# Performance work log

Hardware: AMD Instinct MI355X
Metric: run time of the kernel (lower is better)

The kernel has to match this reference:

```python
import jax, jax.numpy as jnp
import numpy as np

B, S = 4, 8192
DIM, H = 1024, 8
C = 2 * H           # num_channels
E = DIM // C        # head_dim = 64
BASE, START, STRIDE = 10.0, 0, 1
CHUNK = 64
EPS = 1e-8
TWO_PI = 2.0 * np.pi


def setup_inputs() -> dict:
    key = jax.random.key(0)
    k1, k2, k3, k4, k5 = jax.random.split(key, 5)
    inputs = jax.random.normal(k1, (B, S, DIM), jnp.float32)
    timestamps = jnp.sort(jax.random.randint(k2, (B, S), 0, 8192, jnp.int32), axis=-1)
    next_timestamps = jnp.sort(jax.random.randint(k3, (B, S), 0, 8192, jnp.int32), axis=-1)
    mask = jnp.ones((B, S), dtype=bool)
    # learned parameters
    Wv = jax.random.normal(k4, (DIM, DIM), jnp.float32) / np.sqrt(DIM)  # proj_v.weight
    gamma_param = jnp.zeros((H,), jnp.float32)
    alpha = jax.random.normal(k5, (C,), jnp.float32) * 0.02
    beta = jnp.ones((C,), jnp.float32)
    return {"inputs": inputs, "Wv": Wv, "gamma_param": gamma_param, "alpha": alpha,
            "beta": beta, "timestamps": timestamps, "next_timestamps": next_timestamps,
            "mask": mask}


def chunkwise_recurrent_attention(q, k, v, decay_steps, mask, chunk):
    # q,k: [B,S,C,2]; v: [B,S,C,E]; decay_steps: [B,S,C]; mask: [B,S] bool
    b, s, c, d = q.shape
    e = v.shape[-1]
    m4 = mask[..., None, None].astype(q.dtype)
    q = q * m4
    k = k * m4
    v = v * m4
    decay = jnp.where(mask[..., None], decay_steps, jnp.ones_like(decay_steps))
    n = s // chunk

    def chunks(x):  # [B,S,...] -> [n,B,L,...]
        return x.reshape(b, n, chunk, *x.shape[2:]).swapaxes(0, 1)

    qc, kc, vc = chunks(q), chunks(k), chunks(v)
    dc = chunks(decay)                       # [n,B,L,C]
    mc = mask.reshape(b, n, chunk).swapaxes(0, 1)
    causal = jnp.tril(jnp.ones((chunk, chunk), q.dtype))

    def step(state, xs):
        qch, kch, vch, dch, mch = xs         # [B,L,C,2],[B,L,C,2],[B,L,C,E],[B,L,C],[B,L]
        prefix = jnp.cumprod(jnp.clip(dch, EPS), axis=1)            # [B,L,C]
        prev = jnp.einsum('blcd,bcde->blce', qch * prefix[..., None], state)
        dmat = prefix[:, :, None, :] / jnp.clip(prefix[:, None, :, :], EPS)  # [B,L,M,C]
        scores = jnp.einsum('blcd,bmcd->blmc', qch, kch)            # [B,L,M,C]
        weights = scores * dmat * causal[None, :, :, None]
        intra = jnp.einsum('blmc,bmce->blce', weights, vch)
        out = (prev + intra) * mch[..., None, None].astype(qch.dtype)
        plast = prefix[:, -1]                                       # [B,C]
        sw = plast[:, None, :] / jnp.clip(prefix, EPS)              # [B,L,C]
        new_state = state * plast[:, :, None, None] + \
            jnp.einsum('blcd,blce->bcde', kch * sw[..., None], vch)
        return new_state, out

    state0 = jnp.zeros((b, c, d, e), q.dtype)
    _, outs = jax.lax.scan(step, state0, (qc, kc, vc, dc, mc))
    return outs.swapaxes(0, 1).reshape(b, s, c, e)


def _forward(inputs, Wv, gamma_param, alpha, beta, timestamps, next_timestamps, mask):
    values = (inputs @ Wv.T).reshape(B, S, C, E)
    scales = jnp.arange(START, START + H * STRIDE, STRIDE, dtype=jnp.float32)
    intervals = jnp.power(BASE, scales).astype(jnp.int32).astype(jnp.float32)  # buffer cast to long
    scale_factor = TWO_PI * jnp.power(1.0 / BASE, scales)
    ts = timestamps.astype(jnp.float32)
    nts = next_timestamps.astype(jnp.float32)
    theta_k = jnp.remainder(ts[..., None], intervals) * scale_factor   # [B,S,H]
    theta_q = jnp.remainder(nts[..., None], intervals) * scale_factor
    key_ = jnp.stack((jnp.cos(theta_k), jnp.sin(theta_k)), axis=-1)    # [B,S,H,2]
    key_ = jnp.concatenate([key_, key_], axis=2)                       # [B,S,C,2]
    cos_q, sin_q = jnp.cos(theta_q), jnp.sin(theta_q)
    query = jnp.concatenate([jnp.stack((sin_q, -cos_q), -1),
                             jnp.stack((cos_q, sin_q), -1)], axis=2)   # [B,S,C,2]
    gamma = jax.nn.sigmoid(gamma_param)
    loggamma = jnp.log(jnp.clip(gamma, 1e-6))
    delta = jnp.clip(nts - ts, 0.0)
    q_decay = jnp.exp(loggamma * (delta[..., None] * scale_factor))    # [B,S,H]
    q_decay = jnp.concatenate([q_decay, q_decay], axis=-1)             # [B,S,C]
    query = query * q_decay[..., None]
    step_delta = jnp.concatenate(
        [jnp.zeros((B, 1), jnp.float32), jnp.clip(ts[:, 1:] - ts[:, :-1], 0.0)], axis=1)
    decay_steps = jnp.exp(loggamma * (step_delta[..., None] * scale_factor))
    decay_steps = jnp.concatenate([decay_steps, decay_steps], axis=-1)  # [B,S,C]
    out = chunkwise_recurrent_attention(query, key_, values, decay_steps, mask, CHUNK)
    out = out * alpha[None, None, :, None] + values * beta[None, None, :, None]
    return out.reshape(B, S, DIM)


def reference(inputs, Wv, gamma_param, alpha, beta, timestamps, next_timestamps, mask):
    return _forward(inputs, Wv, gamma_param, alpha, beta, timestamps, next_timestamps, mask)
```

## Files before the change

kernel.cpp:

```cpp
#include <hip/hip_runtime.h>
#include <stdint.h>

#define SS   8192
#define DIMD 1024
#define NCH  128
#define CC   16
#define EPSF 1e-8f

typedef __bf16 bh;
typedef bh    bhx4 __attribute__((ext_vector_type(4)));
typedef bh    bhx8 __attribute__((ext_vector_type(8)));
typedef float fx4  __attribute__((ext_vector_type(4)));
typedef unsigned int u32x2 __attribute__((ext_vector_type(2)));

#define GLOAD_LDS16(g, l) __builtin_amdgcn_global_load_lds(                    \
    (const __attribute__((address_space(1))) uint32_t*)(g),                    \
    (__attribute__((address_space(3))) uint32_t*)(l), 16, 0, 0)

#define LDSA(p) ((uint32_t)(uintptr_t)(const __attribute__((address_space(3))) char*)(const char*)(p))

#define SB() __builtin_amdgcn_sched_barrier(0)
#define PRE_BAR()  do { SB(); __builtin_amdgcn_s_barrier(); SB();              \
                        __builtin_amdgcn_s_setprio(1); } while (0)
#define POST_BAR() do { __builtin_amdgcn_s_setprio(0); SB();                   \
                        __builtin_amdgcn_s_barrier(); SB(); } while (0)

__global__ __launch_bounds__(256) void cvt2_k(const float* __restrict__ srcA,
                                              const float* __restrict__ srcW,
                                              bh* __restrict__ dstA,
                                              bh* __restrict__ dstW) {
    const int i = blockIdx.x * 256 + threadIdx.x;
    const float* src;
    bh* dst;
    int idx;
    if (i < 131072) { src = srcW; dst = dstW; idx = i; }
    else            { src = srcA; dst = dstA; idx = i - 131072; }
    const float4 a = reinterpret_cast<const float4*>(src)[idx * 2];
    const float4 b = reinterpret_cast<const float4*>(src)[idx * 2 + 1];
    bhx8 o;
    o[0] = (bh)a.x; o[1] = (bh)a.y; o[2] = (bh)a.z; o[3] = (bh)a.w;
    o[4] = (bh)b.x; o[5] = (bh)b.y; o[6] = (bh)b.z; o[7] = (bh)b.w;
    reinterpret_cast<bhx8*>(dst)[idx] = o;
}

template <typename VT>
__global__ __launch_bounds__(512, 2) void gemm256a(const bh* __restrict__ A,
                                                   const bh* __restrict__ Bw,
                                                   VT* __restrict__ C,
                                                   const int* __restrict__ tsp,
                                                   const float* __restrict__ gammap,
                                                   float* __restrict__ Aws,
                                                   float* __restrict__ plastWs) {
    __shared__ __align__(16) char ldsraw[131072];
    const int lb = blockIdx.x;
    const int logical = (lb & 7) * 64 + (lb >> 3);
    const int mt = logical >> 2;
    const int nt = logical & 3;
    const int tid = threadIdx.x, lane = tid & 63, w = tid >> 6;
    const int wm = w >> 2, wn = w & 3;

    fx4 acc[8][4];
#pragma unroll
    for (int i = 0; i < 8; ++i)
#pragma unroll
        for (int j = 0; j < 4; ++j)
#pragma unroll
            for (int r = 0; r < 4; ++r) acc[i][j][r] = 0.f;

    const int kgo = ((tid & 3) ^ ((tid >> 3) & 3)) << 3;
    const bh* gA0 = A  + (size_t)(mt * 256 + (tid >> 2)) * DIMD + kgo;
    const bh* gB0 = Bw + (size_t)(nt * 256 + (tid >> 2)) * DIMD + kgo;

#define STAGE_U(kt, obase, g, h)                                               \
    { char* lp = ldsraw + ((((kt) & 1) * 65536) + (obase) + (h) * 16384) + tid * 16; \
      const bh* gp = (g) + (kt) * 64 + (h) * 32;                               \
      GLOAD_LDS16(gp, lp);                                                     \
      GLOAD_LDS16(gp + 131072, lp + 8192); }

    const int rAb = wm * 128 + (lane & 15);
    const int rBb = wn * 64 + (lane & 15);
    const int s_swz = (lane >> 4) ^ (((lane & 15) >> 1) & 3);
    const int offA = rAb * 64 + s_swz * 16;
    const int offB = rBb * 64 + s_swz * 16;

    STAGE_U(0, 0, gA0, 0); STAGE_U(0, 32768, gB0, 0);
    STAGE_U(0, 0, gA0, 1); STAGE_U(0, 32768, gB0, 1);
    STAGE_U(1, 0, gA0, 0); STAGE_U(1, 32768, gB0, 0);
    STAGE_U(1, 0, gA0, 1); STAGE_U(1, 32768, gB0, 1);
    asm volatile("s_waitcnt vmcnt(8)" ::: "memory");
    SB(); __builtin_amdgcn_s_barrier(); SB();

#pragma unroll 2
    for (int t = 0; t < 16; ++t) {
        const int buf = t & 1;
        const char* pA0 = ldsraw + buf * 65536 + offA;
        const char* pB0 = ldsraw + buf * 65536 + 32768 + offB;
        bhx8 fa[4], fb[4];

#pragma unroll
        for (int i = 0; i < 4; ++i) fa[i] = *reinterpret_cast<const bhx8*>(pA0 + i * 1024);
#pragma unroll
        for (int j = 0; j < 4; ++j) fb[j] = *reinterpret_cast<const bhx8*>(pB0 + j * 1024);
        if (t >= 1 && t <= 14) STAGE_U(t + 1, 0, gA0, 1);
        PRE_BAR();
#pragma unroll
        for (int i = 0; i < 4; ++i)
#pragma unroll
            for (int j = 0; j < 4; ++j)
                acc[i][j] = __builtin_amdgcn_mfma_f32_16x16x32_bf16(fa[i], fb[j], acc[i][j], 0, 0, 0);
        POST_BAR();

#pragma unroll
        for (int i = 0; i < 4; ++i) fa[i] = *reinterpret_cast<const bhx8*>(pA0 + (4 + i) * 1024);
        if (t <= 13) STAGE_U(t + 2, 32768, gB0, 0);
        PRE_BAR();
#pragma unroll
        for (int i = 0; i < 4; ++i)
#pragma unroll
            for (int j = 0; j < 4; ++j)
                acc[4 + i][j] = __builtin_amdgcn_mfma_f32_16x16x32_bf16(fa[i], fb[j], acc[4 + i][j], 0, 0, 0);
        POST_BAR();

#pragma unroll
        for (int i = 0; i < 4; ++i) fa[i] = *reinterpret_cast<const bhx8*>(pA0 + 16384 + i * 1024);
#pragma unroll
        for (int j = 0; j < 4; ++j) fb[j] = *reinterpret_cast<const bhx8*>(pB0 + 16384 + j * 1024);
        if (t <= 13) STAGE_U(t + 2, 0, gA0, 0);
        PRE_BAR();
#pragma unroll
        for (int i = 0; i < 4; ++i)
#pragma unroll
            for (int j = 0; j < 4; ++j)
                acc[i][j] = __builtin_amdgcn_mfma_f32_16x16x32_bf16(fa[i], fb[j], acc[i][j], 0, 0, 0);
        POST_BAR();

#pragma unroll
        for (int i = 0; i < 4; ++i) fa[i] = *reinterpret_cast<const bhx8*>(pA0 + 16384 + (4 + i) * 1024);
        if (t <= 13) STAGE_U(t + 2, 32768, gB0, 1);
        PRE_BAR();
#pragma unroll
        for (int i = 0; i < 4; ++i)
#pragma unroll
            for (int j = 0; j < 4; ++j)
                acc[4 + i][j] = __builtin_amdgcn_mfma_f32_16x16x32_bf16(fa[i], fb[j], acc[4 + i][j], 0, 0, 0);
        __builtin_amdgcn_s_setprio(0);
        if (t < 14)       { asm volatile("s_waitcnt vmcnt(6)" ::: "memory"); }
        else if (t == 14) { asm volatile("s_waitcnt vmcnt(0)" ::: "memory"); }
        SB(); __builtin_amdgcn_s_barrier(); SB();
    }
#undef STAGE_U

    const int r0 = (lane >> 4) * 4;
    const int c0 = lane & 15;
#pragma unroll
    for (int mi = 0; mi < 8; ++mi) {
#pragma unroll
        for (int ni = 0; ni < 4; ++ni) {
            const size_t m = (size_t)(mt * 256 + wm * 128 + mi * 16 + r0);
            const int    n = nt * 256 + wn * 64 + ni * 16 + c0;
#pragma unroll
            for (int r = 0; r < 4; ++r) {
                if constexpr (sizeof(VT) == 2)
                    C[(m + r) * DIMD + n] = (bh)acc[mi][ni][r];
                else
                    C[(m + r) * DIMD + n] = acc[mi][ni][r];
            }
        }
    }

    float* wlds = (float*)ldsraw + w * 256;
    const int b_ = mt >> 5;
    const int j0 = (mt & 31) * 4;
    const int c_ = nt * 4 + wn;
    const int h_ = c_ & 7;
    float iv = 1.f; double invb = 1.0;
    for (int i = 0; i < h_; i++) { iv *= 10.f; invb *= 0.1; }
    const float sf = (float)(6.283185307179586 * invb);
    const float gm = 1.f / (1.f + expf(-gammap[h_]));
    const float lg = logf(fmaxf(gm, 1e-6f));

#pragma unroll
    for (int jl = 0; jl < 2; ++jl) {
        const int jg = j0 + wm * 2 + jl;
        const int sl = jg * 64 + lane;
        const int its = tsp[b_ * SS + sl];
        const int itp = (sl > 0) ? tsp[b_ * SS + sl - 1] : its;
        int dstep = its - itp; if (dstep < 0) dstep = 0;
        const float dec = expf(lg * ((float)dstep * sf));
        float p = fmaxf(dec, EPSF);
#pragma unroll
        for (int off = 1; off < 64; off <<= 1) {
            float o = __shfl_up(p, off, 64);
            if (lane >= off) p *= o;
        }
        const float plast = __shfl(p, 63, 64);
        const float swv = plast / fmaxf(p, EPSF);
        const float tk = fmodf((float)its, iv) * sf;
        wlds[jl * 128 + lane]      = cosf(tk) * swv;
        wlds[jl * 128 + 64 + lane] = sinf(tk) * swv;
        if (lane == 0) plastWs[(size_t)(b_ * CC + c_) * NCH + jg] = plast;
    }
    asm volatile("s_waitcnt lgkmcnt(0)" ::: "memory");

#pragma unroll
    for (int jl = 0; jl < 2; ++jl) {
        const int jg = j0 + wm * 2 + jl;
        float* ab = Aws + ((size_t)(b_ * CC + c_) * NCH + jg) * 128;
        fx4 w0q[4], w1q[4];
        const int gb = ((lane >> 4) << 2);
#pragma unroll
        for (int q = 0; q < 4; ++q) {
            w0q[q] = *reinterpret_cast<const fx4*>(&wlds[jl * 128 + q * 16 + gb]);
            w1q[q] = *reinterpret_cast<const fx4*>(&wlds[jl * 128 + 64 + q * 16 + gb]);
        }
#pragma unroll
        for (int ni = 0; ni < 4; ++ni) {
            float pa0 = 0.f, pa1 = 0.f;
#pragma unroll
            for (int q = 0; q < 4; ++q)
#pragma unroll
                for (int r = 0; r < 4; ++r) {
                    const float av = acc[jl * 4 + q][ni][r];
                    pa0 += w0q[q][r] * av;
                    pa1 += w1q[q][r] * av;
                }
            pa0 += __shfl_xor(pa0, 16, 64); pa0 += __shfl_xor(pa0, 32, 64);
            pa1 += __shfl_xor(pa1, 16, 64); pa1 += __shfl_xor(pa1, 32, 64);
            const int e = ni * 16 + (lane & 15);
            const int grp = lane >> 4;
            if (grp == 0)      ab[e] = pa0;
            else if (grp == 1) ab[64 + e] = pa1;
        }
    }
}

__global__ __launch_bounds__(256) void gemm_k(const float* __restrict__ Ain,
                                              const float* __restrict__ Win,
                                              float* __restrict__ Cout) {
    __shared__ __align__(16) char ldsraw[20480];
    char* ldsA = ldsraw;
    char* ldsB = ldsraw + 10240;
    const int tid = threadIdx.x;
    const int lane = tid & 63;
    const int w = tid >> 6;
    const int wm = w >> 1, wn = w & 1;
    const int bid = blockIdx.x;
    const int mt = bid >> 3;
    const int nt = bid & 7;
    const size_t Abase = (size_t)mt * 128 * 1024;
    const size_t Bbase = (size_t)nt * 128 * 1024;
    fx4 acc[4][4];
#pragma unroll
    for (int i = 0; i < 4; i++)
#pragma unroll
        for (int j2 = 0; j2 < 4; j2++)
#pragma unroll
            for (int r = 0; r < 4; r++) acc[i][j2][r] = 0.f;
    const int srow0 = tid >> 3;
    const int sc16 = tid & 7;
    for (int kt = 0; kt < 32; ++kt) {
        const int k0 = kt * 32;
#pragma unroll
        for (int jj = 0; jj < 4; jj++) {
            int row = srow0 + jj * 32;
            const float4 va = *reinterpret_cast<const float4*>(Ain + Abase + (size_t)row * 1024 + k0 + sc16 * 4);
            const float4 vb = *reinterpret_cast<const float4*>(Win + Bbase + (size_t)row * 1024 + k0 + sc16 * 4);
            bhx4 ba, bb2;
            ba[0] = (bh)va.x; ba[1] = (bh)va.y; ba[2] = (bh)va.z; ba[3] = (bh)va.w;
            bb2[0] = (bh)vb.x; bb2[1] = (bh)vb.y; bb2[2] = (bh)vb.z; bb2[3] = (bh)vb.w;
            *reinterpret_cast<bhx4*>(ldsA + row * 80 + sc16 * 8) = ba;
            *reinterpret_cast<bhx4*>(ldsB + row * 80 + sc16 * 8) = bb2;
        }
        __syncthreads();
        bhx8 fa[4], fb[4];
        const int kb = (lane >> 4) * 16;
        const int rA = wm * 64 + (lane & 15);
        const int rB = wn * 64 + (lane & 15);
#pragma unroll
        for (int mi = 0; mi < 4; mi++) fa[mi] = *reinterpret_cast<const bhx8*>(ldsA + (rA + mi * 16) * 80 + kb);
#pragma unroll
        for (int ni = 0; ni < 4; ni++) fb[ni] = *reinterpret_cast<const bhx8*>(ldsB + (rB + ni * 16) * 80 + kb);
#pragma unroll
        for (int mi = 0; mi < 4; mi++)
#pragma unroll
            for (int ni = 0; ni < 4; ni++)
                acc[mi][ni] = __builtin_amdgcn_mfma_f32_16x16x32_bf16(fa[mi], fb[ni], acc[mi][ni], 0, 0, 0);
        __syncthreads();
    }
    const int r0 = (lane >> 4) * 4;
    const int cc0 = lane & 15;
#pragma unroll
    for (int mi = 0; mi < 4; mi++) {
#pragma unroll
        for (int ni = 0; ni < 4; ni++) {
            size_t rr = (size_t)(mt * 128 + wm * 64 + mi * 16 + r0);
            int cc = nt * 128 + wn * 64 + ni * 16 + cc0;
#pragma unroll
            for (int r = 0; r < 4; r++) Cout[(rr + r) * 1024 + cc] = acc[mi][ni][r];
        }
    }
}

template <typename VT>
__global__ __launch_bounds__(64) void ka_k(const int* __restrict__ ts,
                                           const float* __restrict__ gammap,
                                           const VT* values,
                                           float* __restrict__ Aws,
                                           float* __restrict__ plastWs) {
    __shared__ float s_k0[64], s_k1[64];
    int bid = blockIdx.x;
    int j = bid & 127;
    int h = (bid >> 7) & 7;
    int b = bid >> 10;
    int l = threadIdx.x;
    int s = j * 64 + l;
    float iv = 1.f; double invb = 1.0;
    for (int i = 0; i < h; i++) { iv *= 10.f; invb *= 0.1; }
    float sf = (float)(6.283185307179586 * invb);
    float gp = gammap[h];
    float gm = 1.f / (1.f + expf(-gp));
    float lg = logf(fmaxf(gm, 1e-6f));
    int its = ts[b * SS + s];
    int itp = (s > 0) ? ts[b * SS + s - 1] : its;
    int dstep = its - itp; if (dstep < 0) dstep = 0;
    float dec = expf(lg * ((float)dstep * sf));
    float p = fmaxf(dec, EPSF);
#pragma unroll
    for (int off = 1; off < 64; off <<= 1) {
        float o = __shfl_up(p, off, 64);
        if (l >= off) p *= o;
    }
    float plast = __shfl(p, 63, 64);
    float swv = plast / fmaxf(p, EPSF);
    float tk = fmodf((float)its, iv) * sf;
    s_k0[l] = cosf(tk) * swv;
    s_k1[l] = sinf(tk) * swv;
    __syncthreads();
    if (l == 0) {
        plastWs[(b * CC + h) * NCH + j] = plast;
        plastWs[(b * CC + h + 8) * NCH + j] = plast;
    }
    int e = l;
#pragma unroll
    for (int cc2 = 0; cc2 < 2; ++cc2) {
        int c = h + cc2 * 8;
        const VT* vb = values + ((size_t)b * SS + (size_t)j * 64) * DIMD + c * 64 + e;
        float a0 = 0.f, a1 = 0.f;
#pragma unroll 8
        for (int m = 0; m < 64; ++m) {
            float vv = (float)vb[(size_t)m * DIMD];
            a0 += s_k0[m] * vv;
            a1 += s_k1[m] * vv;
        }
        float* ab = Aws + ((size_t)(b * CC + c) * NCH + j) * 128;
        ab[e] = a0;
        ab[64 + e] = a1;
    }
}

__global__ __launch_bounds__(128) void kb_k(const float* __restrict__ Aws,
                                            const float* __restrict__ plastWs,
                                            float* __restrict__ Sws) {
    __shared__ float pl[NCH];
    __shared__ __align__(16) float sa[NCH][128];
    const int bc = blockIdx.x;
    const int t = threadIdx.x;
    const int wv = t >> 6;
    const int ln = t & 63;
    pl[t] = plastWs[bc * NCH + t];
    const float* ab = Aws + (size_t)bc * NCH * 128;
#pragma unroll
    for (int i = 0; i < 32; ++i) {
        const int row = i * 4 + wv * 2;
        GLOAD_LDS16(ab + (size_t)row * 128 + ln * 4, (char*)&sa[row][0] + ln * 16);
    }
    asm volatile("s_waitcnt vmcnt(0)" ::: "memory");
    __syncthreads();
    float st = 0.f;
    float* sb = Sws + (size_t)bc * NCH * 128 + t;
#pragma unroll 4
    for (int j = 0; j < NCH; ++j) {
        sb[(size_t)j * 128] = st;
        st = st * pl[j] + sa[j][t];
    }
}

__global__ __launch_bounds__(256, 2) void kc2_k(const int* __restrict__ ts,
                                                const int* __restrict__ nts,
                                                const float* __restrict__ gammap,
                                                const float* __restrict__ alphap,
                                                const float* __restrict__ betap,
                                                const bh* __restrict__ values,
                                                const float* __restrict__ Sws,
                                                float* __restrict__ outp) {
    __shared__ __align__(16) bh vt[8][4096];
    __shared__ float s_b0[4][64], s_b1[4][64];
    __shared__ float s_a0[8][64], s_a1[8][64];
    __shared__ float s_st0[8][64], s_st1[8][64];

    const int bid = blockIdx.x;
    const int g = bid & 1;
    const int j = (bid >> 1) & 127;
    const int b = bid >> 8;
    const int tid = threadIdx.x, lane = tid & 63, w = tid >> 6;
    const int h = g * 4 + w;
    const int s = j * 64 + lane;

    const int its = ts[b * SS + s];
    const int itp = (s > 0) ? ts[b * SS + s - 1] : its;
    const int inx = nts[b * SS + s];
    const float* swp0 = Sws + ((size_t)(b * CC + h) * NCH + j) * 128;
    const float* swp1 = Sws + ((size_t)(b * CC + h + 8) * NCH + j) * 128;
    const float st00 = swp0[lane], st10 = swp0[64 + lane];
    const float st01 = swp1[lane], st11 = swp1[64 + lane];
    const float al0 = alphap[h], al1 = alphap[h + 8];
    const float be0 = betap[h], be1 = betap[h + 8];
    const float gp = gammap[h];

    const bh* gv0 = values + ((size_t)b * SS + (size_t)j * 64 + (lane >> 1)) * DIMD
                    + h * 64 + (lane & 1) * 8;
    const bh* gv1 = gv0 + 512;
    char* lc0 = (char*)&vt[w * 2][0] + lane * 16;
    char* lc1 = (char*)&vt[w * 2 + 1][0] + lane * 16;
#pragma unroll
    for (int mh = 0; mh < 2; ++mh)
#pragma unroll
        for (int pp = 0; pp < 4; ++pp)
            GLOAD_LDS16(gv0 + mh * 32 * DIMD + pp * 16, lc0 + pp * 2048 + mh * 1024);
#pragma unroll
    for (int mh = 0; mh < 2; ++mh)
#pragma unroll
        for (int pp = 0; pp < 4; ++pp)
            GLOAD_LDS16(gv1 + mh * 32 * DIMD + pp * 16, lc1 + pp * 2048 + mh * 1024);

    float iv = 1.f; double invb = 1.0;
    for (int i = 0; i < h; i++) { iv *= 10.f; invb *= 0.1; }
    const float sf = (float)(6.283185307179586 * invb);
    const float gm = 1.f / (1.f + expf(-gp));
    const float lg = logf(fmaxf(gm, 1e-6f));
    int dstep = its - itp; if (dstep < 0) dstep = 0;
    const float dec = expf(lg * ((float)dstep * sf));
    float p = fmaxf(dec, EPSF);
#pragma unroll
    for (int off = 1; off < 64; off <<= 1) {
        float o = __shfl_up(p, off, 64);
        if (lane >= off) p *= o;
    }
    const float ipv = 1.f / fmaxf(p, EPSF);
    const float tk = fmodf((float)its, iv) * sf;
    const float k0 = cosf(tk), k1 = sinf(tk);
    s_b0[w][lane] = k0 * ipv;
    s_b1[w][lane] = k1 * ipv;
    const float tq = fmodf((float)inx, iv) * sf;
    int dq = inx - its; if (dq < 0) dq = 0;
    const float qd = expf(lg * ((float)dq * sf));
    const float sq = sinf(tq), cq = cosf(tq);
    const int r0i = w * 2, r1i = w * 2 + 1;
    s_a0[r0i][lane] = sq * qd * p * al0;  s_a1[r0i][lane] = -cq * qd * p * al0;
    s_a0[r1i][lane] = cq * qd * p * al1;  s_a1[r1i][lane] = sq * qd * p * al1;
    s_st0[r0i][lane] = st00; s_st1[r0i][lane] = st10;
    s_st0[r1i][lane] = st01; s_st1[r1i][lane] = st11;
    asm volatile("s_waitcnt lgkmcnt(0)" ::: "memory");

    fx4 rb0[2][2], rb1[2][2];
#pragma unroll
    for (int ks = 0; ks < 2; ++ks) {
        const int m0 = ks * 32 + (lane >> 4) * 8;
        rb0[ks][0] = *reinterpret_cast<const fx4*>(&s_b0[w][m0]);
        rb0[ks][1] = *reinterpret_cast<const fx4*>(&s_b0[w][m0 + 4]);
        rb1[ks][0] = *reinterpret_cast<const fx4*>(&s_b1[w][m0]);
        rb1[ks][1] = *reinterpret_cast<const fx4*>(&s_b1[w][m0 + 4]);
    }

#pragma unroll
    for (int cc = 0; cc < 2; ++cc) {
        const int reg = w * 2 + cc;
        const int c = h + cc * 8;
        const char* vbase2 = (const char*)&vt[reg][0];

        bhx8 pa[4][2];
#pragma unroll
        for (int mi = 0; mi < 4; ++mi) {
            const int l = mi * 16 + (lane & 15);
            const float a0l = s_a0[reg][l];
            const float a1l = s_a1[reg][l];
#pragma unroll
            for (int ks = 0; ks < 2; ++ks) {
                if (mi * 16 + 16 <= ks * 32) continue;
                const bool full = (mi * 16 >= ks * 32 + 32);
                bhx8 v;
#pragma unroll
                for (int jj = 0; jj < 8; ++jj) {
                    const int m = ks * 32 + (lane >> 4) * 8 + jj;
                    const float b0m = rb0[ks][jj >> 2][jj & 3];
                    const float b1m = rb1[ks][jj >> 2][jj & 3];
                    const float val = a0l * b0m + a1l * b1m;
                    v[jj] = (full || l >= m) ? (bh)val : (bh)0.f;
                }
                pa[mi][ks] = v;
            }
        }

        if (cc == 0) { asm volatile("s_waitcnt vmcnt(8)" ::: "memory"); }
        else         { asm volatile("s_waitcnt vmcnt(0)" ::: "memory"); }

        const uint32_t tb = LDSA(vbase2) + ((lane >> 4) << 8) + ((lane & 15) << 3);
        bhx8 pb[4][2];
#pragma unroll
        for (int ni = 0; ni < 4; ++ni)
#pragma unroll
            for (int ks = 0; ks < 2; ++ks) {
                const uint32_t a2 = tb + ni * 2048 + ks * 1024;
                u32x2 lo, hi;
                asm volatile("ds_read_b64_tr_b16 %0, %2 offset:0\n\t"
                             "ds_read_b64_tr_b16 %1, %2 offset:128"
                             : "=&v"(lo), "=&v"(hi) : "v"(a2));
                union { u32x2 u[2]; bhx8 f; } u_;
                u_.u[0] = lo; u_.u[1] = hi;
                pb[ni][ks] = u_.f;
            }
        asm volatile("s_waitcnt lgkmcnt(0)" ::: "memory");
        SB();

        fx4 acc[4][4];
#pragma unroll
        for (int mi = 0; mi < 4; ++mi)
#pragma unroll
            for (int ni = 0; ni < 4; ++ni)
#pragma unroll
                for (int r = 0; r < 4; ++r) acc[mi][ni][r] = 0.f;
        __builtin_amdgcn_s_setprio(1);
#pragma unroll
        for (int ks = 0; ks < 2; ++ks)
#pragma unroll
            for (int mi = 0; mi < 4; ++mi) {
                if (mi * 16 + 16 <= ks * 32) continue;
#pragma unroll
                for (int ni = 0; ni < 4; ++ni)
                    acc[mi][ni] = __builtin_amdgcn_mfma_f32_16x16x32_bf16(
                        pa[mi][ks], pb[ni][ks], acc[mi][ni], 0, 0, 0);
            }
        __builtin_amdgcn_s_setprio(0);
        SB();

        float st0e[4], st1e[4];
#pragma unroll
        for (int ni = 0; ni < 4; ++ni) {
            st0e[ni] = s_st0[reg][ni * 16 + (lane & 15)];
            st1e[ni] = s_st1[reg][ni * 16 + (lane & 15)];
        }
        const float bev = (cc == 0) ? be0 : be1;
        float* ob = outp + ((size_t)b * SS + (size_t)j * 64) * DIMD + c * 64 + (lane & 15);
#pragma unroll
        for (int mi = 0; mi < 4; ++mi)
#pragma unroll
            for (int r = 0; r < 4; ++r) {
                const int l = mi * 16 + ((lane >> 4) << 2) + r;
                const float a0l = s_a0[reg][l];
                const float a1l = s_a1[reg][l];
#pragma unroll
                for (int ni = 0; ni < 4; ++ni) {
                    const float vv = (float)*reinterpret_cast<const bh*>(
                        vbase2 + ni * 2048 + (mi * 4 + (lane >> 4)) * 128 + r * 32 + ((lane & 15) << 1));
                    const float o = acc[mi][ni][r] + a0l * st0e[ni] + a1l * st1e[ni] + bev * vv;
                    ob[(size_t)l * DIMD + ni * 16] = o;
                }
            }
    }
}

template <typename VT>
__global__ __launch_bounds__(256) void kc_k(const int* __restrict__ ts,
                                            const int* __restrict__ nts,
                                            const float* __restrict__ gammap,
                                            const float* __restrict__ alphap,
                                            const float* __restrict__ betap,
                                            const VT* values,
                                            const float* __restrict__ Sws,
                                            float* outp) {
    __shared__ float vsm[64][64];
    __shared__ float s_p[64], s_ip[64], s_k0[64], s_k1[64], s_q0[64], s_q1[64];
    __shared__ float s_st[128];
    int bid = blockIdx.x;
    int j = bid & 127;
    int c = (bid >> 7) & 15;
    int b = bid >> 11;
    int h = c & 7;
    int tid = threadIdx.x;
    if (tid < 64) {
        int l = tid;
        int s = j * 64 + l;
        float iv = 1.f; double invb = 1.0;
        for (int i = 0; i < h; i++) { iv *= 10.f; invb *= 0.1; }
        float sf = (float)(6.283185307179586 * invb);
        float gp = gammap[h];
        float gm = 1.f / (1.f + expf(-gp));
        float lg = logf(fmaxf(gm, 1e-6f));
        int its = ts[b * SS + s];
        int itp = (s > 0) ? ts[b * SS + s - 1] : its;
        int dstep = its - itp; if (dstep < 0) dstep = 0;
        float dec = expf(lg * ((float)dstep * sf));
        float p = fmaxf(dec, EPSF);
#pragma unroll
        for (int off = 1; off < 64; off <<= 1) {
            float o = __shfl_up(p, off, 64);
            if (l >= off) p *= o;
        }
        s_p[l] = p;
        s_ip[l] = 1.f / fmaxf(p, EPSF);
        float tk = fmodf((float)its, iv) * sf;
        s_k0[l] = cosf(tk);
        s_k1[l] = sinf(tk);
        int inx = nts[b * SS + s];
        float tq = fmodf((float)inx, iv) * sf;
        int dq = inx - its; if (dq < 0) dq = 0;
        float qd = expf(lg * ((float)dq * sf));
        float sq = sinf(tq), cq2 = cosf(tq);
        s_q0[l] = (c < 8) ? sq * qd : cq2 * qd;
        s_q1[l] = (c < 8) ? (-cq2 * qd) : sq * qd;
    }
    const VT* vbase = values + ((size_t)b * SS + (size_t)j * 64) * DIMD + c * 64;
#pragma unroll
    for (int i = 0; i < 2; ++i) {
        int f = tid + i * 256;
        int row = f >> 3;
        int c8 = f & 7;
        if constexpr (sizeof(VT) == 2) {
            bhx8 v8 = *reinterpret_cast<const bhx8*>(vbase + (size_t)row * DIMD + c8 * 8);
#pragma unroll
            for (int r = 0; r < 8; ++r) vsm[row][c8 * 8 + r] = (float)v8[r];
        } else {
            *reinterpret_cast<float4*>(&vsm[row][c8 * 8]) =
                *reinterpret_cast<const float4*>(vbase + (size_t)row * DIMD + c8 * 8);
            *reinterpret_cast<float4*>(&vsm[row][c8 * 8 + 4]) =
                *reinterpret_cast<const float4*>(vbase + (size_t)row * DIMD + c8 * 8 + 4);
        }
    }
    if (tid < 128) {
        s_st[tid] = Sws[((size_t)(b * CC + c) * NCH + j) * 128 + tid];
    }
    __syncthreads();
    int l = tid >> 2, eg = tid & 3;
    float acc[16];
#pragma unroll
    for (int i = 0; i < 16; i++) acc[i] = 0.f;
    float q0 = s_q0[l], q1 = s_q1[l], pl_ = s_p[l];
    for (int m = 0; m <= l; ++m) {
        float wgt = (q0 * s_k0[m] + q1 * s_k1[m]) * (pl_ * s_ip[m]);
        const float* vr = &vsm[m][eg * 16];
#pragma unroll
        for (int i = 0; i < 16; i++) acc[i] += wgt * vr[i];
    }
    float al = alphap[c], be = betap[c];
    float* ob = outp + ((size_t)b * SS + (size_t)j * 64 + l) * DIMD + c * 64 + eg * 16;
    const float* st0 = &s_st[eg * 16];
    const float* st1 = &s_st[64 + eg * 16];
#pragma unroll
    for (int i2 = 0; i2 < 4; i2++) {
        float4 vv = *reinterpret_cast<const float4*>(&vsm[l][eg * 16 + i2 * 4]);
        float4 o4;
        const float* vvp = (const float*)&vv;
        float* o4p = (float*)&o4;
#pragma unroll
        for (int r = 0; r < 4; r++) {
            int i = i2 * 4 + r;
            float prevt = pl_ * (q0 * st0[i] + q1 * st1[i]);
            o4p[r] = (prevt + acc[i]) * al + vvp[r] * be;
        }
        *reinterpret_cast<float4*>(ob + i2 * 4) = o4;
    }
}

extern "C" void kernel_launch(void* const* d_in, const int* in_sizes, int n_in,
                              void* d_out, int out_size, void* d_ws, size_t ws_size,
                              hipStream_t stream) {
    const float* inputs = (const float*)d_in[0];
    const float* Wv     = (const float*)d_in[1];
    const float* gammap = (const float*)d_in[2];
    const float* alphap = (const float*)d_in[3];
    const float* betap  = (const float*)d_in[4];
    const int*   ts     = (const int*)d_in[5];
    const int*   nts    = (const int*)d_in[6];
    float* outp = (float*)d_out;
    char* ws = (char*)d_ws;

    float* Aws     = (float*)ws;
    float* plastWs = (float*)(ws + 4194304);
    float* Sws     = (float*)(ws + 4227072);
    const size_t base   = 8421376;
    const size_t abytes = 67108864;
    const size_t wbytes = 2097152;
    const size_t vbytes = 67108864;

    if (ws_size >= base + abytes + wbytes + vbytes) {
        bh* Abf = (bh*)(ws + base);
        bh* Wbf = (bh*)(ws + base + abytes);
        bh* Vbf = (bh*)(ws + base + abytes + wbytes);
        cvt2_k<<<16896, 256, 0, stream>>>(inputs, Wv, Abf, Wbf);
        gemm256a<bh><<<512, 512, 0, stream>>>(Abf, Wbf, Vbf, ts, gammap, Aws, plastWs);
        kb_k<<<64, 128, 0, stream>>>(Aws, plastWs, Sws);
        kc2_k<<<1024, 256, 0, stream>>>(ts, nts, gammap, alphap, betap, Vbf, Sws, outp);
    } else if (ws_size >= base + abytes + wbytes) {
        bh* Abf = (bh*)(ws + base);
        bh* Wbf = (bh*)(ws + base + abytes);
        cvt2_k<<<16896, 256, 0, stream>>>(inputs, Wv, Abf, Wbf);
        gemm256a<float><<<512, 512, 0, stream>>>(Abf, Wbf, outp, ts, gammap, Aws, plastWs);
        kb_k<<<64, 128, 0, stream>>>(Aws, plastWs, Sws);
        kc_k<float><<<8192, 256, 0, stream>>>(ts, nts, gammap, alphap, betap, outp, Sws, outp);
    } else {
        gemm_k<<<2048, 256, 0, stream>>>(inputs, Wv, outp);
        ka_k<float><<<4096, 64, 0, stream>>>(ts, gammap, outp, Aws, plastWs);
        kb_k<<<64, 128, 0, stream>>>(Aws, plastWs, Sws);
        kc_k<float><<<8192, 256, 0, stream>>>(ts, nts, gammap, alphap, betap, outp, Sws, outp);
    }
}
```

Measured before the change: 170.2 us.

## Fold beta*v residual into MFMA and stage output through LDS for vector stores

Adds the beta*values residual term through extra MFMAs that multiply a scaled identity fragment by the already-loaded V operand, removing per-element scalar bf16 reads from LDS. The epilogue writes the accumulator tile into a swizzled LDS scratch area, reusing the V tile buffer, and then issues 16-byte coalesced global stores instead of scattered 4-byte stores. This costs extra MFMA work and LDS round trips with waits. Reusing the vt buffer as scratch relies on the V tile no longer being needed by the other waves at that point.

New measurement: 168.3 us. No clear change (-1.1%).

```diff
diff --git a/kernel.cpp b/kernel.cpp
--- a/kernel.cpp
+++ b/kernel.cpp
@@ -472,11 +472,15 @@
         rb1[ks][1] = *reinterpret_cast<const fx4*>(&s_b1[w][m0 + 4]);
     }
 
+    char* scr = (char*)&vt[w * 2][0];
+    const size_t bSSj = (size_t)b * SS + (size_t)j * 64;
+
 #pragma unroll
     for (int cc = 0; cc < 2; ++cc) {
         const int reg = w * 2 + cc;
         const int c = h + cc * 8;
         const char* vbase2 = (const char*)&vt[reg][0];
+        const float bev = (cc == 0) ? be0 : be1;
 
         bhx8 pa[4][2];
 #pragma unroll
@@ -499,6 +503,17 @@
                 }
                 pa[mi][ks] = v;
             }
+        }
+
+        bhx8 idf[2];
+#pragma unroll
+        for (int me = 0; me < 2; ++me) {
+            bhx8 z;
+#pragma unroll
+            for (int jj = 0; jj < 8; ++jj) z[jj] = (bh)0.f;
+            const int jj = (lane & 15) + me * 16 - (lane >> 4) * 8;
+            if (jj >= 0 && jj < 8) z[jj] = (bh)bev;
+            idf[me] = z;
         }
 
         if (cc == 0) { asm volatile("s_waitcnt vmcnt(8)" ::: "memory"); }
@@ -540,6 +555,14 @@
                     acc[mi][ni] = __builtin_amdgcn_mfma_f32_16x16x32_bf16(
                         pa[mi][ks], pb[ni][ks], acc[mi][ni], 0, 0, 0);
             }
+#pragma unroll
+        for (int mi = 0; mi < 4; ++mi) {
+            const int ks = mi >> 1;
+#pragma unroll
+            for (int ni = 0; ni < 4; ++ni)
+                acc[mi][ni] = __builtin_amdgcn_mfma_f32_16x16x32_bf16(
+                    idf[mi & 1], pb[ni][ks], acc[mi][ni], 0, 0, 0);
+        }
         __builtin_amdgcn_s_setprio(0);
         SB();
 
@@ -549,8 +572,6 @@
             st0e[ni] = s_st0[reg][ni * 16 + (lane & 15)];
             st1e[ni] = s_st1[reg][ni * 16 + (lane & 15)];
         }
-        const float bev = (cc == 0) ? be0 : be1;
-        float* ob = outp + ((size_t)b * SS + (size_t)j * 64) * DIMD + c * 64 + (lane & 15);
 #pragma unroll
         for (int mi = 0; mi < 4; ++mi)
 #pragma unroll
@@ -559,13 +580,40 @@
                 const float a0l = s_a0[reg][l];
                 const float a1l = s_a1[reg][l];
 #pragma unroll
+                for (int ni = 0; ni < 4; ++ni)
+                    acc[mi][ni][r] += a0l * st0e[ni] + a1l * st1e[ni];
+            }
+
+#pragma unroll
+        for (int mh = 0; mh < 2; ++mh) {
+#pragma unroll
+            for (int mq = 0; mq < 2; ++mq) {
+                const int mi = mh * 2 + mq;
+                const int rlb = mq * 16 + ((lane >> 4) << 2);
+#pragma unroll
                 for (int ni = 0; ni < 4; ++ni) {
-                    const float vv = (float)*reinterpret_cast<const bh*>(
-                        vbase2 + ni * 2048 + (mi * 4 + (lane >> 4)) * 128 + r * 32 + ((lane & 15) << 1));
-                    const float o = acc[mi][ni][r] + a0l * st0e[ni] + a1l * st1e[ni] + bev * vv;
-                    ob[(size_t)l * DIMD + ni * 16] = o;
+                    const int slot = ni * 4 + ((lane & 15) >> 2);
+#pragma unroll
+                    for (int r = 0; r < 4; ++r) {
+                        const int rl = rlb + r;
+                        const int sp = (slot + rl) & 15;
+                        *(float*)(scr + rl * 256 + sp * 16 + (lane & 3) * 4) = acc[mi][ni][r];
+                    }
                 }
             }
+            asm volatile("s_waitcnt lgkmcnt(0)" ::: "memory");
+            SB();
+#pragma unroll
+            for (int i = 0; i < 8; ++i) {
+                const int rr = (lane >> 4) + i * 4;
+                const int sp = ((lane & 15) + rr) & 15;
+                const fx4 v4 = *reinterpret_cast<const fx4*>(scr + rr * 256 + sp * 16);
+                float* op = outp + (bSSj + mh * 32 + rr) * DIMD + c * 64 + (lane & 15) * 4;
+                *reinterpret_cast<fx4*>(op) = v4;
+            }
+            asm volatile("s_waitcnt lgkmcnt(0)" ::: "memory");
+            SB();
+        }
     }
 }
 
```
